# Optimization experiments

Measured on AMD Instinct MI355X. Metric: run time of the kernel, lower is better.

Reference implementation:

```python
import jax, jax.numpy as jnp
import numpy as np

VOCAB, EMB, HID = 32000, 512, 1024
BATCH, SEQ = 32, 512


def setup_inputs() -> dict:
    key = jax.random.key(0)
    ks = jax.random.split(key, 5)
    scale_e = 1.0 / np.sqrt(EMB)
    scale_h = 1.0 / np.sqrt(HID)
    return {
        "source": jax.random.randint(ks[0], (BATCH, SEQ), 0, VOCAB, dtype=jnp.int64),
        "embedding": jax.random.normal(ks[1], (VOCAB, EMB), dtype=jnp.float32),
        "W_ih": jax.random.normal(ks[2], (EMB, 4 * HID), dtype=jnp.float32) * scale_e,
        "W_hh": jax.random.normal(ks[3], (HID, 4 * HID), dtype=jnp.float32) * scale_h,
        "b_ih": jnp.zeros((4 * HID,), dtype=jnp.float32),
        "b_hh": jnp.zeros((4 * HID,), dtype=jnp.float32),
    }


def _lstm_forward(source, embedding, W_ih, W_hh, b_ih, b_hh):
    B, S = source.shape
    H = W_hh.shape[0]
    embedded = embedding[source]                      # [B, S, E]
    # Precompute input contributions for all timesteps in one big GEMM.
    x_gates = jnp.einsum("bse,eg->bsg", embedded, W_ih) + b_ih + b_hh  # [B, S, 4H]

    def step(carry, xg_t):
        h, c = carry
        gates = xg_t + h @ W_hh                       # [B, 4H]
        i, f, g, o = jnp.split(gates, 4, axis=-1)
        i = jax.nn.sigmoid(i)
        f = jax.nn.sigmoid(f)
        g = jnp.tanh(g)
        o = jax.nn.sigmoid(o)
        c_new = f * c + i * g
        h_new = o * jnp.tanh(c_new)
        return (h_new, c_new), h_new

    h0 = jnp.zeros((B, H), dtype=embedded.dtype)
    c0 = jnp.zeros((B, H), dtype=embedded.dtype)
    # scan over time: [S, B, 4H]
    _, hiddens = jax.lax.scan(step, (h0, c0), jnp.swapaxes(x_gates, 0, 1))
    return jnp.swapaxes(hiddens, 0, 1)                # [B, S, H]


def reference(source, embedding, W_ih, W_hh, b_ih, b_hh):
    return _lstm_forward(source, embedding, W_ih, W_hh, b_ih, b_hh)
```

## Files before the change

### kernel.cpp

```cpp
#include <hip/hip_runtime.h>
#include <math.h>


#define B_ 32
#define S_ 512
#define E_ 512
#define H_ 1024
#define G_ 4096
#define NWG 256
#define RTHR 512
#define BH_ (B_ * H_)
#define XGPAD 40

typedef _Float16 f16x8 __attribute__((ext_vector_type(8)));
typedef _Float16 f16x4 __attribute__((ext_vector_type(4)));
typedef float f32x4 __attribute__((ext_vector_type(4)));

__device__ __forceinline__ float sigmoidf_(float x) {
  return 1.0f / (1.0f + __expf(-x));
}
__device__ __forceinline__ float tanhf_(float x) {
  return 1.0f - 2.0f / (__expf(2.0f * x) + 1.0f);
}

__global__ __launch_bounds__(256) void wt_kernel(
    const float* __restrict__ W, _Float16* __restrict__ Wt, int K)
{
  __shared__ float Lt[64][65];
  const int c0 = blockIdx.x * 64;
  const int k0 = blockIdx.y * 64;
  const int tid = threadIdx.x;
  const int colL = tid & 63;
  const int rq = tid >> 6;
#pragma unroll 4
  for (int p = 0; p < 16; ++p) {
    int r = p * 4 + rq;
    Lt[colL][r] = W[(size_t)(k0 + r) * G_ + c0 + colL];
  }
  __syncthreads();
  const int col = tid >> 2;
  const int kq = (tid & 3) * 16;
  _Float16 tmp[16];
#pragma unroll
  for (int i = 0; i < 16; ++i) tmp[i] = (_Float16)Lt[col][kq + i];
  *(f16x8*)(Wt + (size_t)(c0 + col) * K + k0 + kq)     = *(f16x8*)&tmp[0];
  *(f16x8*)(Wt + (size_t)(c0 + col) * K + k0 + kq + 8) = *(f16x8*)&tmp[8];
}

__global__ __launch_bounds__(128) void gather_a(
    const int* __restrict__ src, const float* __restrict__ emb,
    _Float16* __restrict__ A, int t0)
{
  const int r = blockIdx.x;
  const int t = t0 + (r >> 5), b = r & 31;
  const int vrow = src[b * S_ + t];
  const float4 v = *(const float4*)(emb + (size_t)vrow * E_ + threadIdx.x * 4);
  f16x4 o = { (_Float16)v.x, (_Float16)v.y, (_Float16)v.z, (_Float16)v.w };
  *(f16x4*)(A + (size_t)r * E_ + threadIdx.x * 4) = o;
}

__global__ __launch_bounds__(256) void xgates_mfma(
    const _Float16* __restrict__ A, const _Float16* __restrict__ Bw,
    const float* __restrict__ bih, const float* __restrict__ bhh,
    _Float16* __restrict__ xg)
{
  __shared__ _Float16 Al[128][XGPAD];
  __shared__ _Float16 Bl[128][XGPAD];
  const int tid = threadIdx.x;
  const int row0 = blockIdx.y * 128;
  const int col0 = blockIdx.x * 128;
  const int wave = tid >> 6, lane = tid & 63;
  const int wm = wave >> 1, wn = wave & 1;
  const int lrow = lane & 15, lhi = lane >> 4;

  float bias[4];
#pragma unroll
  for (int n = 0; n < 4; ++n) {
    int c = col0 + wn * 64 + n * 16 + lrow;
    bias[n] = bih[c] + bhh[c];
  }
  f32x4 acc[4][4];
#pragma unroll
  for (int m = 0; m < 4; ++m)
#pragma unroll
    for (int n = 0; n < 4; ++n)
      acc[m][n] = (f32x4){bias[n], bias[n], bias[n], bias[n]};

  for (int kt = 0; kt < E_ / 32; ++kt) {
#pragma unroll
    for (int p = 0; p < 2; ++p) {
      int cch = tid * 2 + p;
      int rr = cch >> 2, kc = cch & 3;
      *(f16x8*)&Al[rr][kc * 8] =
          *(const f16x8*)(A + (size_t)(row0 + rr) * E_ + kt * 32 + kc * 8);
      *(f16x8*)&Bl[rr][kc * 8] =
          *(const f16x8*)(Bw + (size_t)(col0 + rr) * E_ + kt * 32 + kc * 8);
    }
    __syncthreads();
    f16x8 af[4], bfr[4];
#pragma unroll
    for (int m = 0; m < 4; ++m)
      af[m] = *(const f16x8*)&Al[wm * 64 + m * 16 + lrow][lhi * 8];
#pragma unroll
    for (int n = 0; n < 4; ++n)
      bfr[n] = *(const f16x8*)&Bl[wn * 64 + n * 16 + lrow][lhi * 8];
#pragma unroll
    for (int m = 0; m < 4; ++m)
#pragma unroll
      for (int n = 0; n < 4; ++n)
        acc[m][n] = __builtin_amdgcn_mfma_f32_16x16x32_f16(af[m], bfr[n],
                                                           acc[m][n], 0, 0, 0);
    __syncthreads();
  }
#pragma unroll
  for (int m = 0; m < 4; ++m)
#pragma unroll
    for (int n = 0; n < 4; ++n) {
      const int ccol = col0 + wn * 64 + n * 16 + lrow;
#pragma unroll
      for (int r = 0; r < 4; ++r) {
        const int rrow = row0 + wm * 64 + m * 16 + lhi * 4 + r;
        xg[(size_t)rrow * G_ + ccol] = (_Float16)acc[m][n][r];
      }
    }
}

__global__ __launch_bounds__(RTHR) void lstm_mfma(
    const _Float16* __restrict__ Wt, const _Float16* __restrict__ xg,
    unsigned short* hring, float* cbuf, unsigned* flg,
    float* out, int t0, int nt)
{
  __shared__ float red[8 * 32 * 17];

  const int wg = blockIdx.x;
  const int tid = threadIdx.x;
  const int J0 = 4 * ((wg & 7) * 32 + (wg >> 3));

  const int wave = tid >> 6;
  const int lane = tid & 63;
  const int lrow = lane & 15;
  const int lhi  = lane >> 4;
  const int Kw   = wave * 128;
  const int gcol = (lrow >> 2) * H_ + J0 + (lrow & 3);

  f16x8 bf[4];
#pragma unroll
  for (int s = 0; s < 4; ++s)
    bf[s] = *(const f16x8*)(Wt + (size_t)gcol * H_ + Kw + s * 32 + lhi * 8);

  const int bq = tid >> 2, jq = tid & 3;
  float cstate = 0.f;
  if (tid < 128) cstate = cbuf[(size_t)bq * H_ + J0 + jq];

  float xv0 = 0.f, xv1 = 0.f, xv2 = 0.f, xv3 = 0.f;
  if (tid < 128) {
    const _Float16* xp = xg + (size_t)bq * G_ + J0 + jq;
    xv0 = (float)xp[0];      xv1 = (float)xp[H_];
    xv2 = (float)xp[2 * H_]; xv3 = (float)xp[3 * H_];
  }

  for (int t = t0; t < t0 + nt; ++t) {
    const int lt = t - t0;
    const _Float16* hrd = (const _Float16*)hring + (size_t)lt * BH_;
    unsigned short* hwr = hring + (size_t)((lt == nt - 1) ? 0 : lt + 1) * BH_;

    if (wave == 0) {
      const unsigned* fp = flg + (size_t)t * 256 + lane * 4;
      int guard = 0;
      for (;;) {
        unsigned a0 = __hip_atomic_load(fp + 0, __ATOMIC_RELAXED, __HIP_MEMORY_SCOPE_AGENT);
        unsigned a1 = __hip_atomic_load(fp + 1, __ATOMIC_RELAXED, __HIP_MEMORY_SCOPE_AGENT);
        unsigned a2 = __hip_atomic_load(fp + 2, __ATOMIC_RELAXED, __HIP_MEMORY_SCOPE_AGENT);
        unsigned a3 = __hip_atomic_load(fp + 3, __ATOMIC_RELAXED, __HIP_MEMORY_SCOPE_AGENT);
        if (__all((a0 & a1 & a2 & a3) != 0u)) break;
        __builtin_amdgcn_s_sleep(1);
        if (++guard > (1 << 22)) break;
      }
    }
    __syncthreads();

    f32x4 acc0 = {0.f, 0.f, 0.f, 0.f};
    f32x4 acc1 = {0.f, 0.f, 0.f, 0.f};
#pragma unroll
    for (int s = 0; s < 4; ++s) {
      f16x8 a0 = *(const f16x8*)(hrd + (size_t)lrow * H_ + Kw + s * 32 + lhi * 8);
      f16x8 a1 = *(const f16x8*)(hrd + (size_t)(16 + lrow) * H_ + Kw + s * 32 + lhi * 8);
      acc0 = __builtin_amdgcn_mfma_f32_16x16x32_f16(a0, bf[s], acc0, 0, 0, 0);
      acc1 = __builtin_amdgcn_mfma_f32_16x16x32_f16(a1, bf[s], acc1, 0, 0, 0);
    }

    float xn0 = 0.f, xn1 = 0.f, xn2 = 0.f, xn3 = 0.f;
    if (tid < 128) {
      const int nlt = (lt == nt - 1) ? lt : lt + 1;
      const _Float16* xp = xg + ((size_t)nlt * B_ + bq) * G_ + J0 + jq;
      xn0 = (float)xp[0];      xn1 = (float)xp[H_];
      xn2 = (float)xp[2 * H_]; xn3 = (float)xp[3 * H_];
    }

#pragma unroll
    for (int r = 0; r < 4; ++r) {
      red[(wave * 32 + lhi * 4 + r) * 17 + lrow]      = acc0[r];
      red[(wave * 32 + 16 + lhi * 4 + r) * 17 + lrow] = acc1[r];
    }
    __syncthreads();

    if (tid < 128) {
      float g0 = xv0, g1 = xv1, g2 = xv2, g3 = xv3;
#pragma unroll
      for (int w = 0; w < 8; ++w) {
        const float* rp = red + (w * 32 + bq) * 17;
        g0 += rp[jq];
        g1 += rp[4 + jq];
        g2 += rp[8 + jq];
        g3 += rp[12 + jq];
      }
      float ig = sigmoidf_(g0);
      float fg = sigmoidf_(g1);
      float gg = tanhf_(g2);
      float og = sigmoidf_(g3);
      cstate = fg * cstate + ig * gg;
      float hval = og * tanhf_(cstate);
      out[((size_t)bq * S_ + t) * H_ + J0 + jq] = hval;
      _Float16 hf = (_Float16)hval;
      unsigned short hb;
      __builtin_memcpy(&hb, &hf, 2);
      __hip_atomic_store(hwr + (size_t)bq * H_ + J0 + jq, hb,
                         __ATOMIC_RELAXED, __HIP_MEMORY_SCOPE_AGENT);
    }
    __syncthreads();

    if (tid == 0)
      __hip_atomic_store(flg + (size_t)(t + 1) * 256 + wg, 1u,
                         __ATOMIC_RELAXED, __HIP_MEMORY_SCOPE_AGENT);

    xv0 = xn0; xv1 = xn1; xv2 = xn2; xv3 = xn3;
  }

  if (tid < 128) cbuf[(size_t)bq * H_ + J0 + jq] = cstate;
}

extern "C" void kernel_launch(void* const* d_in, const int* in_sizes, int n_in,
                              void* d_out, int out_size, void* d_ws, size_t ws_size,
                              hipStream_t stream) {
  const int*   src = (const int*)d_in[0];
  const float* emb = (const float*)d_in[1];
  const float* Wih = (const float*)d_in[2];
  const float* Whh = (const float*)d_in[3];
  const float* bih = (const float*)d_in[4];
  const float* bhh = (const float*)d_in[5];
  float* out = (float*)d_out;

  char* ws = (char*)d_ws;
  float*    cbuf = (float*)ws;
  unsigned* flg  = (unsigned*)(ws + 131072);
  const size_t stateBytes = 131072 + 525312;
  _Float16* Wt  = (_Float16*)(ws + stateBytes);
  _Float16* Wt2 = (_Float16*)(ws + stateBytes + 8388608);
  const size_t fixedBytes = stateBytes + 8388608 + 4194304;

  int chunk = 0;
  const int cand[4] = {512, 256, 128, 64};
  for (int ci = 0; ci < 4; ++ci) {
    size_t need = fixedBytes + (size_t)(cand[ci] + 1) * (BH_ * 2)
                  + (size_t)cand[ci] * B_ * E_ * 2
                  + (size_t)cand[ci] * B_ * G_ * 2;
    if (need <= ws_size) { chunk = cand[ci]; break; }
  }
  if (chunk == 0) return;

  unsigned short* hring = (unsigned short*)(ws + fixedBytes);
  _Float16* Af16 = (_Float16*)(ws + fixedBytes + (size_t)(chunk + 1) * (BH_ * 2));
  _Float16* xg   = (_Float16*)(ws + fixedBytes + (size_t)(chunk + 1) * (BH_ * 2)
                               + (size_t)chunk * B_ * E_ * 2);

  (void)hipMemsetAsync(ws, 0, stateBytes, stream);
  (void)hipMemsetAsync(flg, 1, 1024, stream);
  (void)hipMemsetAsync(hring, 0, BH_ * 2, stream);

  int K1 = H_, K2 = E_;
  wt_kernel<<<dim3(64, 16), 256, 0, stream>>>(Whh, Wt, K1);
  wt_kernel<<<dim3(64, 8), 256, 0, stream>>>(Wih, Wt2, K2);

  for (int t0 = 0; t0 < S_; t0 += chunk) {
    gather_a<<<dim3(chunk * B_), 128, 0, stream>>>(src, emb, Af16, t0);
    xgates_mfma<<<dim3(G_ / 128, chunk * B_ / 128), 256, 0, stream>>>(
        Af16, Wt2, bih, bhh, xg);

    int nt = chunk;
    void* args[] = {(void*)&Wt, (void*)&xg, (void*)&hring, (void*)&cbuf,
                    (void*)&flg, (void*)&out, (void*)&t0, (void*)&nt};
    (void)hipLaunchCooperativeKernel((void*)lstm_mfma, dim3(NWG), dim3(RTHR),
                                     args, 0u, stream);
  }
}
```

Measured before the change: 2.642 ms.

## Restructure recurrent LSTM kernel to per-wave full-K MFMA with wave-level flags

Replaces the 256-workgroup recurrent kernel, which split K across 8 waves and reduced through LDS with three block barriers per step, by a 64-workgroup layout. Each wave now owns a 16-batch by 4-hidden-unit tile over the full K=1024, holds 32 register fragments of W_hh, and combines gates through lane shuffles instead of shared memory. Synchronisation moves to per-wave flags split by batch half, so each wave waits only on the 256 producers of its batch half and signals independently, with no __syncthreads. This trades much higher register pressure and longer serial MFMA chains per wave for removing the block barriers and LDS reduction from the per-step critical path.

```diff
diff --git a/kernel.cpp b/kernel.cpp
--- a/kernel.cpp
+++ b/kernel.cpp
@@ -7,7 +7,7 @@
 #define E_ 512
 #define H_ 1024
 #define G_ 4096
-#define NWG 256
+#define NWG 64
 #define RTHR 512
 #define BH_ (B_ * H_)
 #define XGPAD 40
@@ -125,47 +125,41 @@
     }
 }
 
-__global__ __launch_bounds__(RTHR) void lstm_mfma(
+__global__ __launch_bounds__(RTHR) void lstm_wave(
     const _Float16* __restrict__ Wt, const _Float16* __restrict__ xg,
     unsigned short* hring, float* cbuf, unsigned* flg,
     float* out, int t0, int nt)
 {
-  __shared__ float red[8 * 32 * 17];
-
   const int wg = blockIdx.x;
   const int tid = threadIdx.x;
-  const int J0 = 4 * ((wg & 7) * 32 + (wg >> 3));
-
   const int wave = tid >> 6;
   const int lane = tid & 63;
-  const int lrow = lane & 15;
-  const int lhi  = lane >> 4;
-  const int Kw   = wave * 128;
-  const int gcol = (lrow >> 2) * H_ + J0 + (lrow & 3);
-
-  f16x8 bf[4];
-#pragma unroll
-  for (int s = 0; s < 4; ++s)
-    bf[s] = *(const f16x8*)(Wt + (size_t)gcol * H_ + Kw + s * 32 + lhi * 8);
-
-  const int bq = tid >> 2, jq = tid & 3;
-  float cstate = 0.f;
-  if (tid < 128) cstate = cbuf[(size_t)bq * H_ + J0 + jq];
-
-  float xv0 = 0.f, xv1 = 0.f, xv2 = 0.f, xv3 = 0.f;
-  if (tid < 128) {
-    const _Float16* xp = xg + (size_t)bq * G_ + J0 + jq;
-    xv0 = (float)xp[0];      xv1 = (float)xp[H_];
-    xv2 = (float)xp[2 * H_]; xv3 = (float)xp[3 * H_];
-  }
+  const int lrow = lane & 15, lhi = lane >> 4;
+  const int bt = wave >> 2;
+  const int ct = wave & 3;
+  const int gcol = (lrow >> 2) * H_ + wg * 16 + ct * 4 + (lrow & 3);
+
+  f16x8 bf[32];
+#pragma unroll
+  for (int s = 0; s < 32; ++s)
+    bf[s] = *(const f16x8*)(Wt + (size_t)gcol * H_ + s * 32 + lhi * 8);
+
+  const int ej    = lane & 3;
+  const int ersel = (lane >> 2) & 3;
+  const int ebl   = (lane >> 4) * 4 + ersel;
+  const int eb    = bt * 16 + ebl;
+  const int eu    = wg * 16 + ct * 4 + ej;
+  const int shbase = (lane & 48) | ej;
+
+  float cstate = cbuf[(size_t)eb * H_ + eu];
 
   for (int t = t0; t < t0 + nt; ++t) {
     const int lt = t - t0;
     const _Float16* hrd = (const _Float16*)hring + (size_t)lt * BH_;
     unsigned short* hwr = hring + (size_t)((lt == nt - 1) ? 0 : lt + 1) * BH_;
 
-    if (wave == 0) {
-      const unsigned* fp = flg + (size_t)t * 256 + lane * 4;
+    {
+      const unsigned* fp = flg + (size_t)t * 512 + bt * 256 + lane * 4;
       int guard = 0;
       for (;;) {
         unsigned a0 = __hip_atomic_load(fp + 0, __ATOMIC_RELAXED, __HIP_MEMORY_SCOPE_AGENT);
@@ -174,69 +168,67 @@
         unsigned a3 = __hip_atomic_load(fp + 3, __ATOMIC_RELAXED, __HIP_MEMORY_SCOPE_AGENT);
         if (__all((a0 & a1 & a2 & a3) != 0u)) break;
         __builtin_amdgcn_s_sleep(1);
-        if (++guard > (1 << 22)) break;
+        if (++guard > (1 << 20)) break;
       }
     }
-    __syncthreads();
-
-    f32x4 acc0 = {0.f, 0.f, 0.f, 0.f};
-    f32x4 acc1 = {0.f, 0.f, 0.f, 0.f};
-#pragma unroll
-    for (int s = 0; s < 4; ++s) {
-      f16x8 a0 = *(const f16x8*)(hrd + (size_t)lrow * H_ + Kw + s * 32 + lhi * 8);
-      f16x8 a1 = *(const f16x8*)(hrd + (size_t)(16 + lrow) * H_ + Kw + s * 32 + lhi * 8);
-      acc0 = __builtin_amdgcn_mfma_f32_16x16x32_f16(a0, bf[s], acc0, 0, 0, 0);
-      acc1 = __builtin_amdgcn_mfma_f32_16x16x32_f16(a1, bf[s], acc1, 0, 0, 0);
-    }
-
-    float xn0 = 0.f, xn1 = 0.f, xn2 = 0.f, xn3 = 0.f;
-    if (tid < 128) {
-      const int nlt = (lt == nt - 1) ? lt : lt + 1;
-      const _Float16* xp = xg + ((size_t)nlt * B_ + bq) * G_ + J0 + jq;
-      xn0 = (float)xp[0];      xn1 = (float)xp[H_];
-      xn2 = (float)xp[2 * H_]; xn3 = (float)xp[3 * H_];
-    }
-
-#pragma unroll
-    for (int r = 0; r < 4; ++r) {
-      red[(wave * 32 + lhi * 4 + r) * 17 + lrow]      = acc0[r];
-      red[(wave * 32 + 16 + lhi * 4 + r) * 17 + lrow] = acc1[r];
-    }
-    __syncthreads();
-
-    if (tid < 128) {
-      float g0 = xv0, g1 = xv1, g2 = xv2, g3 = xv3;
-#pragma unroll
-      for (int w = 0; w < 8; ++w) {
-        const float* rp = red + (w * 32 + bq) * 17;
-        g0 += rp[jq];
-        g1 += rp[4 + jq];
-        g2 += rp[8 + jq];
-        g3 += rp[12 + jq];
-      }
-      float ig = sigmoidf_(g0);
-      float fg = sigmoidf_(g1);
-      float gg = tanhf_(g2);
-      float og = sigmoidf_(g3);
-      cstate = fg * cstate + ig * gg;
-      float hval = og * tanhf_(cstate);
-      out[((size_t)bq * S_ + t) * H_ + J0 + jq] = hval;
-      _Float16 hf = (_Float16)hval;
-      unsigned short hb;
-      __builtin_memcpy(&hb, &hf, 2);
-      __hip_atomic_store(hwr + (size_t)bq * H_ + J0 + jq, hb,
-                         __ATOMIC_RELAXED, __HIP_MEMORY_SCOPE_AGENT);
-    }
-    __syncthreads();
-
-    if (tid == 0)
-      __hip_atomic_store(flg + (size_t)(t + 1) * 256 + wg, 1u,
-                         __ATOMIC_RELAXED, __HIP_MEMORY_SCOPE_AGENT);
-
-    xv0 = xn0; xv1 = xn1; xv2 = xn2; xv3 = xn3;
-  }
-
-  if (tid < 128) cbuf[(size_t)bq * H_ + J0 + jq] = cstate;
+
+    const _Float16* xp = xg + ((size_t)lt * B_ + eb) * G_ + eu;
+    const float x0 = (float)xp[0];
+    const float x1 = (float)xp[H_];
+    const float x2 = (float)xp[2 * H_];
+    const float x3 = (float)xp[3 * H_];
+
+    const _Float16* hp = hrd + (size_t)(bt * 16 + lrow) * H_ + lhi * 8;
+    f32x4 acA = {0.f, 0.f, 0.f, 0.f};
+    f32x4 acB = {0.f, 0.f, 0.f, 0.f};
+#pragma unroll
+    for (int sb = 0; sb < 8; ++sb) {
+      f16x8 a0 = *(const f16x8*)(hp + (sb * 4 + 0) * 32);
+      f16x8 a1 = *(const f16x8*)(hp + (sb * 4 + 1) * 32);
+      f16x8 a2 = *(const f16x8*)(hp + (sb * 4 + 2) * 32);
+      f16x8 a3 = *(const f16x8*)(hp + (sb * 4 + 3) * 32);
+      acA = __builtin_amdgcn_mfma_f32_16x16x32_f16(a0, bf[sb * 4 + 0], acA, 0, 0, 0);
+      acB = __builtin_amdgcn_mfma_f32_16x16x32_f16(a1, bf[sb * 4 + 1], acB, 0, 0, 0);
+      acA = __builtin_amdgcn_mfma_f32_16x16x32_f16(a2, bf[sb * 4 + 2], acA, 0, 0, 0);
+      acB = __builtin_amdgcn_mfma_f32_16x16x32_f16(a3, bf[sb * 4 + 3], acB, 0, 0, 0);
+    }
+    const float av0 = acA[0] + acB[0];
+    const float av1 = acA[1] + acB[1];
+    const float av2 = acA[2] + acB[2];
+    const float av3 = acA[3] + acB[3];
+
+    float gv[4];
+#pragma unroll
+    for (int g = 0; g < 4; ++g) {
+      const int srcl = shbase + g * 4;
+      const float t0v = __shfl(av0, srcl);
+      const float t1v = __shfl(av1, srcl);
+      const float t2v = __shfl(av2, srcl);
+      const float t3v = __shfl(av3, srcl);
+      gv[g] = (ersel == 0) ? t0v : (ersel == 1) ? t1v : (ersel == 2) ? t2v : t3v;
+    }
+
+    const float ig = sigmoidf_(x0 + gv[0]);
+    const float fg = sigmoidf_(x1 + gv[1]);
+    const float gg = tanhf_(x2 + gv[2]);
+    const float og = sigmoidf_(x3 + gv[3]);
+    cstate = fg * cstate + ig * gg;
+    const float hval = og * tanhf_(cstate);
+
+    out[((size_t)eb * S_ + t) * H_ + eu] = hval;
+    const _Float16 hf = (_Float16)hval;
+    unsigned short hb;
+    __builtin_memcpy(&hb, &hf, 2);
+    __hip_atomic_store(hwr + (size_t)eb * H_ + eu, hb,
+                       __ATOMIC_RELAXED, __HIP_MEMORY_SCOPE_AGENT);
+
+    asm volatile("s_waitcnt vmcnt(0)" ::: "memory");
+    if (lane == 0)
+      __hip_atomic_store(flg + (size_t)(t + 1) * 512 + bt * 256 + wg * 4 + ct,
+                         1u, __ATOMIC_RELAXED, __HIP_MEMORY_SCOPE_AGENT);
+  }
+
+  cbuf[(size_t)eb * H_ + eu] = cstate;
 }
 
 extern "C" void kernel_launch(void* const* d_in, const int* in_sizes, int n_in,
@@ -253,7 +245,7 @@
   char* ws = (char*)d_ws;
   float*    cbuf = (float*)ws;
   unsigned* flg  = (unsigned*)(ws + 131072);
-  const size_t stateBytes = 131072 + 525312;
+  const size_t stateBytes = 131072 + 1050624;
   _Float16* Wt  = (_Float16*)(ws + stateBytes);
   _Float16* Wt2 = (_Float16*)(ws + stateBytes + 8388608);
   const size_t fixedBytes = stateBytes + 8388608 + 4194304;
@@ -274,7 +266,7 @@
                                + (size_t)chunk * B_ * E_ * 2);
 
   (void)hipMemsetAsync(ws, 0, stateBytes, stream);
-  (void)hipMemsetAsync(flg, 1, 1024, stream);
+  (void)hipMemsetAsync(flg, 1, 2048, stream);
   (void)hipMemsetAsync(hring, 0, BH_ * 2, stream);
 
   int K1 = H_, K2 = E_;
@@ -289,7 +281,7 @@
     int nt = chunk;
     void* args[] = {(void*)&Wt, (void*)&xg, (void*)&hring, (void*)&cbuf,
                     (void*)&flg, (void*)&out, (void*)&t0, (void*)&nt};
-    (void)hipLaunchCooperativeKernel((void*)lstm_mfma, dim3(NWG), dim3(RTHR),
+    (void)hipLaunchCooperativeKernel((void*)lstm_wave, dim3(NWG), dim3(RTHR),
                                      args, 0u, stream);
   }
 }
```

Measured after the change: 9.898 ms. 275% more time.

## Replace per-step flag barrier with step-tagged hidden-state values in double buffer

Applied to the files above, without the earlier changes.

The recurrent kernel no longer uses a separate flag array and spin on per-workgroup flags. Instead each hidden value is stored as a 32-bit word carrying the fp16 value plus the timestep tag, in a two-slot buffer. Consumers spin directly on the data they need until every tag matches the current step. The work split also changes: each workgroup now handles 16 batch rows by 8 units rather than 32 rows by 4 units. This removes one flag round-trip and two block barriers per step, and lets the reads that confirm readiness double as the operand loads. In exchange each hidden load is twice as wide, and every lane polls 16 atomic words.

```diff
diff --git a/kernel.cpp b/kernel.cpp
--- a/kernel.cpp
+++ b/kernel.cpp
@@ -15,12 +15,16 @@
 typedef _Float16 f16x8 __attribute__((ext_vector_type(8)));
 typedef _Float16 f16x4 __attribute__((ext_vector_type(4)));
 typedef float f32x4 __attribute__((ext_vector_type(4)));
+typedef unsigned long long u64;
 
 __device__ __forceinline__ float sigmoidf_(float x) {
   return 1.0f / (1.0f + __expf(-x));
 }
 __device__ __forceinline__ float tanhf_(float x) {
   return 1.0f - 2.0f / (__expf(2.0f * x) + 1.0f);
+}
+__device__ __forceinline__ unsigned pack_(u64 q) {
+  return (unsigned)(q & 0xFFFFu) | ((unsigned)(q >> 16) & 0xFFFF0000u);
 }
 
 __global__ __launch_bounds__(256) void wt_kernel(
@@ -125,118 +129,133 @@
     }
 }
 
-__global__ __launch_bounds__(RTHR) void lstm_mfma(
+#define LDQ(i) q##i = __hip_atomic_load(                                    \
+    hq + (((i) >> 2) * 16 + ((i) & 3)), __ATOMIC_RELAXED,                   \
+    __HIP_MEMORY_SCOPE_AGENT);
+#define XOR8(a,b,c,d,e,f,g,h) (((a)|(b))|((c)|(d)))|(((e)|(f))|((g)|(h)))
+
+__global__ __launch_bounds__(RTHR, 2) void lstm_tag(
     const _Float16* __restrict__ Wt, const _Float16* __restrict__ xg,
-    unsigned short* hring, float* cbuf, unsigned* flg,
-    float* out, int t0, int nt)
+    unsigned* hbuf, float* cbuf, float* out, int t0, int nt)
 {
-  __shared__ float red[8 * 32 * 17];
+  __shared__ float red[2][8][16][33];
 
   const int wg = blockIdx.x;
   const int tid = threadIdx.x;
-  const int J0 = 4 * ((wg & 7) * 32 + (wg >> 3));
+  const int bt = wg >> 7;
+  const int ug = wg & 127;
+  const int U0 = ug * 8;
 
   const int wave = tid >> 6;
   const int lane = tid & 63;
-  const int lrow = lane & 15;
-  const int lhi  = lane >> 4;
-  const int Kw   = wave * 128;
-  const int gcol = (lrow >> 2) * H_ + J0 + (lrow & 3);
-
-  f16x8 bf[4];
-#pragma unroll
-  for (int s = 0; s < 4; ++s)
-    bf[s] = *(const f16x8*)(Wt + (size_t)gcol * H_ + Kw + s * 32 + lhi * 8);
-
-  const int bq = tid >> 2, jq = tid & 3;
+  const int lrow = lane & 15, lhi = lane >> 4;
+  const int kq = wave;
+
+  f16x8 bfr[2][4];
+#pragma unroll
+  for (int ct = 0; ct < 2; ++ct) {
+    const int c = ct * 16 + lrow;
+    const int gcol = (c >> 3) * H_ + U0 + (c & 7);
+#pragma unroll
+    for (int s = 0; s < 4; ++s)
+      bfr[ct][s] = *(const f16x8*)(Wt + (size_t)gcol * H_ + kq * 128 + s * 32 + lhi * 8);
+  }
+
+  const int bl = tid >> 3, ej = tid & 7;
+  const int eb = bt * 16 + bl;
+  const int eu = U0 + ej;
   float cstate = 0.f;
-  if (tid < 128) cstate = cbuf[(size_t)bq * H_ + J0 + jq];
+  if (tid < 128) cstate = cbuf[(size_t)eb * H_ + eu];
 
   float xv0 = 0.f, xv1 = 0.f, xv2 = 0.f, xv3 = 0.f;
   if (tid < 128) {
-    const _Float16* xp = xg + (size_t)bq * G_ + J0 + jq;
+    const _Float16* xp = xg + (size_t)eb * G_ + eu;
     xv0 = (float)xp[0];      xv1 = (float)xp[H_];
     xv2 = (float)xp[2 * H_]; xv3 = (float)xp[3 * H_];
   }
 
+  const size_t rowOff64 = (size_t)(bt * 16 + lrow) * (H_ / 2) + kq * 64 + lhi * 4;
+
   for (int t = t0; t < t0 + nt; ++t) {
     const int lt = t - t0;
-    const _Float16* hrd = (const _Float16*)hring + (size_t)lt * BH_;
-    unsigned short* hwr = hring + (size_t)((lt == nt - 1) ? 0 : lt + 1) * BH_;
-
-    if (wave == 0) {
-      const unsigned* fp = flg + (size_t)t * 256 + lane * 4;
+    const int slot = t & 1, nslot = slot ^ 1;
+    const u64* hq = (const u64*)hbuf + (size_t)slot * (BH_ / 2) + rowOff64;
+
+    u64 q0, q1, q2, q3, q4, q5, q6, q7, q8, q9, q10, q11, q12, q13, q14, q15;
+    {
+      const u64 expect = ((u64)(unsigned)t << 16) | ((u64)(unsigned)t << 48);
       int guard = 0;
       for (;;) {
-        unsigned a0 = __hip_atomic_load(fp + 0, __ATOMIC_RELAXED, __HIP_MEMORY_SCOPE_AGENT);
-        unsigned a1 = __hip_atomic_load(fp + 1, __ATOMIC_RELAXED, __HIP_MEMORY_SCOPE_AGENT);
-        unsigned a2 = __hip_atomic_load(fp + 2, __ATOMIC_RELAXED, __HIP_MEMORY_SCOPE_AGENT);
-        unsigned a3 = __hip_atomic_load(fp + 3, __ATOMIC_RELAXED, __HIP_MEMORY_SCOPE_AGENT);
-        if (__all((a0 & a1 & a2 & a3) != 0u)) break;
+        LDQ(0)  LDQ(1)  LDQ(2)  LDQ(3)  LDQ(4)  LDQ(5)  LDQ(6)  LDQ(7)
+        LDQ(8)  LDQ(9)  LDQ(10) LDQ(11) LDQ(12) LDQ(13) LDQ(14) LDQ(15)
+        const u64 bad =
+            (XOR8(q0 ^ expect, q1 ^ expect, q2 ^ expect, q3 ^ expect,
+                  q4 ^ expect, q5 ^ expect, q6 ^ expect, q7 ^ expect) |
+             XOR8(q8 ^ expect, q9 ^ expect, q10 ^ expect, q11 ^ expect,
+                  q12 ^ expect, q13 ^ expect, q14 ^ expect, q15 ^ expect)) &
+            0xFFFF0000FFFF0000ULL;
+        if (__all(bad == 0ULL)) break;
         __builtin_amdgcn_s_sleep(1);
-        if (++guard > (1 << 22)) break;
+        if (++guard > (1 << 20)) break;
       }
     }
-    __syncthreads();
 
     f32x4 acc0 = {0.f, 0.f, 0.f, 0.f};
     f32x4 acc1 = {0.f, 0.f, 0.f, 0.f};
-#pragma unroll
-    for (int s = 0; s < 4; ++s) {
-      f16x8 a0 = *(const f16x8*)(hrd + (size_t)lrow * H_ + Kw + s * 32 + lhi * 8);
-      f16x8 a1 = *(const f16x8*)(hrd + (size_t)(16 + lrow) * H_ + Kw + s * 32 + lhi * 8);
-      acc0 = __builtin_amdgcn_mfma_f32_16x16x32_f16(a0, bf[s], acc0, 0, 0, 0);
-      acc1 = __builtin_amdgcn_mfma_f32_16x16x32_f16(a1, bf[s], acc1, 0, 0, 0);
-    }
-
-    float xn0 = 0.f, xn1 = 0.f, xn2 = 0.f, xn3 = 0.f;
-    if (tid < 128) {
-      const int nlt = (lt == nt - 1) ? lt : lt + 1;
-      const _Float16* xp = xg + ((size_t)nlt * B_ + bq) * G_ + J0 + jq;
-      xn0 = (float)xp[0];      xn1 = (float)xp[H_];
-      xn2 = (float)xp[2 * H_]; xn3 = (float)xp[3 * H_];
-    }
+#define KSTEP(s, qa, qb, qc, qd)                                              \
+    {                                                                         \
+      unsigned pu[4] = { pack_(qa), pack_(qb), pack_(qc), pack_(qd) };        \
+      f16x8 av;                                                               \
+      __builtin_memcpy(&av, pu, 16);                                          \
+      acc0 = __builtin_amdgcn_mfma_f32_16x16x32_f16(av, bfr[0][s], acc0, 0, 0, 0); \
+      acc1 = __builtin_amdgcn_mfma_f32_16x16x32_f16(av, bfr[1][s], acc1, 0, 0, 0); \
+    }
+    KSTEP(0, q0, q1, q2, q3)
+    KSTEP(1, q4, q5, q6, q7)
+    KSTEP(2, q8, q9, q10, q11)
+    KSTEP(3, q12, q13, q14, q15)
+#undef KSTEP
 
 #pragma unroll
     for (int r = 0; r < 4; ++r) {
-      red[(wave * 32 + lhi * 4 + r) * 17 + lrow]      = acc0[r];
-      red[(wave * 32 + 16 + lhi * 4 + r) * 17 + lrow] = acc1[r];
+      red[slot][kq][lhi * 4 + r][lrow]      = acc0[r];
+      red[slot][kq][lhi * 4 + r][16 + lrow] = acc1[r];
     }
     __syncthreads();
 
     if (tid < 128) {
       float g0 = xv0, g1 = xv1, g2 = xv2, g3 = xv3;
 #pragma unroll
-      for (int w = 0; w < 8; ++w) {
-        const float* rp = red + (w * 32 + bq) * 17;
-        g0 += rp[jq];
-        g1 += rp[4 + jq];
-        g2 += rp[8 + jq];
-        g3 += rp[12 + jq];
+      for (int k8 = 0; k8 < 8; ++k8) {
+        const float* rp = &red[slot][k8][bl][0];
+        g0 += rp[ej];
+        g1 += rp[8 + ej];
+        g2 += rp[16 + ej];
+        g3 += rp[24 + ej];
       }
-      float ig = sigmoidf_(g0);
-      float fg = sigmoidf_(g1);
-      float gg = tanhf_(g2);
-      float og = sigmoidf_(g3);
+      const float ig = sigmoidf_(g0);
+      const float fg = sigmoidf_(g1);
+      const float gg = tanhf_(g2);
+      const float og = sigmoidf_(g3);
       cstate = fg * cstate + ig * gg;
-      float hval = og * tanhf_(cstate);
-      out[((size_t)bq * S_ + t) * H_ + J0 + jq] = hval;
-      _Float16 hf = (_Float16)hval;
+      const float hval = og * tanhf_(cstate);
+
+      const _Float16 hf = (_Float16)hval;
       unsigned short hb;
       __builtin_memcpy(&hb, &hf, 2);
-      __hip_atomic_store(hwr + (size_t)bq * H_ + J0 + jq, hb,
+      const unsigned hu = ((unsigned)(t + 1) << 16) | (unsigned)hb;
+      __hip_atomic_store(hbuf + (size_t)nslot * BH_ + (size_t)eb * H_ + eu, hu,
                          __ATOMIC_RELAXED, __HIP_MEMORY_SCOPE_AGENT);
-    }
-    __syncthreads();
-
-    if (tid == 0)
-      __hip_atomic_store(flg + (size_t)(t + 1) * 256 + wg, 1u,
-                         __ATOMIC_RELAXED, __HIP_MEMORY_SCOPE_AGENT);
-
-    xv0 = xn0; xv1 = xn1; xv2 = xn2; xv3 = xn3;
-  }
-
-  if (tid < 128) cbuf[(size_t)bq * H_ + J0 + jq] = cstate;
+      out[((size_t)eb * S_ + t) * H_ + eu] = hval;
+
+      const int nlt = (lt == nt - 1) ? lt : lt + 1;
+      const _Float16* xp = xg + ((size_t)nlt * B_ + eb) * G_ + eu;
+      xv0 = (float)xp[0];      xv1 = (float)xp[H_];
+      xv2 = (float)xp[2 * H_]; xv3 = (float)xp[3 * H_];
+    }
+  }
+
+  if (tid < 128) cbuf[(size_t)eb * H_ + eu] = cstate;
 }
 
 extern "C" void kernel_launch(void* const* d_in, const int* in_sizes, int n_in,
@@ -252,8 +271,8 @@
 
   char* ws = (char*)d_ws;
   float*    cbuf = (float*)ws;
-  unsigned* flg  = (unsigned*)(ws + 131072);
-  const size_t stateBytes = 131072 + 525312;
+  unsigned* hbuf = (unsigned*)(ws + 131072);
+  const size_t stateBytes = 131072 + 262144;
   _Float16* Wt  = (_Float16*)(ws + stateBytes);
   _Float16* Wt2 = (_Float16*)(ws + stateBytes + 8388608);
   const size_t fixedBytes = stateBytes + 8388608 + 4194304;
@@ -261,21 +280,16 @@
   int chunk = 0;
   const int cand[4] = {512, 256, 128, 64};
   for (int ci = 0; ci < 4; ++ci) {
-    size_t need = fixedBytes + (size_t)(cand[ci] + 1) * (BH_ * 2)
-                  + (size_t)cand[ci] * B_ * E_ * 2
+    size_t need = fixedBytes + (size_t)cand[ci] * B_ * E_ * 2
                   + (size_t)cand[ci] * B_ * G_ * 2;
     if (need <= ws_size) { chunk = cand[ci]; break; }
   }
   if (chunk == 0) return;
 
-  unsigned short* hring = (unsigned short*)(ws + fixedBytes);
-  _Float16* Af16 = (_Float16*)(ws + fixedBytes + (size_t)(chunk + 1) * (BH_ * 2));
-  _Float16* xg   = (_Float16*)(ws + fixedBytes + (size_t)(chunk + 1) * (BH_ * 2)
-                               + (size_t)chunk * B_ * E_ * 2);
+  _Float16* Af16 = (_Float16*)(ws + fixedBytes);
+  _Float16* xg   = (_Float16*)(ws + fixedBytes + (size_t)chunk * B_ * E_ * 2);
 
   (void)hipMemsetAsync(ws, 0, stateBytes, stream);
-  (void)hipMemsetAsync(flg, 1, 1024, stream);
-  (void)hipMemsetAsync(hring, 0, BH_ * 2, stream);
 
   int K1 = H_, K2 = E_;
   wt_kernel<<<dim3(64, 16), 256, 0, stream>>>(Whh, Wt, K1);
@@ -287,9 +301,9 @@
         Af16, Wt2, bih, bhh, xg);
 
     int nt = chunk;
-    void* args[] = {(void*)&Wt, (void*)&xg, (void*)&hring, (void*)&cbuf,
-                    (void*)&flg, (void*)&out, (void*)&t0, (void*)&nt};
-    (void)hipLaunchCooperativeKernel((void*)lstm_mfma, dim3(NWG), dim3(RTHR),
+    void* args[] = {(void*)&Wt, (void*)&xg, (void*)&hbuf, (void*)&cbuf,
+                    (void*)&out, (void*)&t0, (void*)&nt};
+    (void)hipLaunchCooperativeKernel((void*)lstm_tag, dim3(NWG), dim3(RTHR),
                                      args, 0u, stream);
   }
 }
```

Measured after the change: 5.486 ms. 2.08x slower.

## Split recurrent LSTM work by batch halves to narrow cross-workgroup flag waits

Applied to the files above, without the earlier changes.

Each workgroup now handles 16 batch rows and 8 hidden units (32 gate columns), not all 32 batch rows and 4 hidden units. This lets each workgroup wait only on the 128 flags of its own batch half instead of all 256. The W_hh fragments held in registers double, but each wave loads one h fragment per k-step and reuses it across two MFMAs. The next-step x-gate prefetch is also moved to after the h store, which shortens the critical path between flag wait and flag publish.

```diff
diff --git a/kernel.cpp b/kernel.cpp
--- a/kernel.cpp
+++ b/kernel.cpp
@@ -125,36 +125,43 @@
     }
 }
 
-__global__ __launch_bounds__(RTHR) void lstm_mfma(
+__global__ __launch_bounds__(RTHR) void lstm_half(
     const _Float16* __restrict__ Wt, const _Float16* __restrict__ xg,
     unsigned short* hring, float* cbuf, unsigned* flg,
     float* out, int t0, int nt)
 {
-  __shared__ float red[8 * 32 * 17];
+  __shared__ float red[8][16][33];
 
   const int wg = blockIdx.x;
   const int tid = threadIdx.x;
-  const int J0 = 4 * ((wg & 7) * 32 + (wg >> 3));
+  const int ht  = wg >> 7;
+  const int rem = wg & 127;
+  const int U0  = 8 * ((rem & 7) * 16 + (rem >> 3));
 
   const int wave = tid >> 6;
   const int lane = tid & 63;
-  const int lrow = lane & 15;
-  const int lhi  = lane >> 4;
-  const int Kw   = wave * 128;
-  const int gcol = (lrow >> 2) * H_ + J0 + (lrow & 3);
-
-  f16x8 bf[4];
-#pragma unroll
-  for (int s = 0; s < 4; ++s)
-    bf[s] = *(const f16x8*)(Wt + (size_t)gcol * H_ + Kw + s * 32 + lhi * 8);
-
-  const int bq = tid >> 2, jq = tid & 3;
+  const int lrow = lane & 15, lhi = lane >> 4;
+  const int kq = wave;
+
+  f16x8 bfr[2][4];
+#pragma unroll
+  for (int ct = 0; ct < 2; ++ct) {
+    const int c = ct * 16 + lrow;
+    const int gcol = (c >> 3) * H_ + U0 + (c & 7);
+#pragma unroll
+    for (int s = 0; s < 4; ++s)
+      bfr[ct][s] = *(const f16x8*)(Wt + (size_t)gcol * H_ + kq * 128 + s * 32 + lhi * 8);
+  }
+
+  const int bl = tid >> 3, ej = tid & 7;
+  const int eb = ht * 16 + bl;
+  const int eu = U0 + ej;
   float cstate = 0.f;
-  if (tid < 128) cstate = cbuf[(size_t)bq * H_ + J0 + jq];
+  if (tid < 128) cstate = cbuf[(size_t)eb * H_ + eu];
 
   float xv0 = 0.f, xv1 = 0.f, xv2 = 0.f, xv3 = 0.f;
   if (tid < 128) {
-    const _Float16* xp = xg + (size_t)bq * G_ + J0 + jq;
+    const _Float16* xp = xg + (size_t)eb * G_ + eu;
     xv0 = (float)xp[0];      xv1 = (float)xp[H_];
     xv2 = (float)xp[2 * H_]; xv3 = (float)xp[3 * H_];
   }
@@ -165,78 +172,74 @@
     unsigned short* hwr = hring + (size_t)((lt == nt - 1) ? 0 : lt + 1) * BH_;
 
     if (wave == 0) {
-      const unsigned* fp = flg + (size_t)t * 256 + lane * 4;
+      const unsigned* fp = flg + (size_t)t * 256 + ht * 128 + lane;
       int guard = 0;
       for (;;) {
-        unsigned a0 = __hip_atomic_load(fp + 0, __ATOMIC_RELAXED, __HIP_MEMORY_SCOPE_AGENT);
-        unsigned a1 = __hip_atomic_load(fp + 1, __ATOMIC_RELAXED, __HIP_MEMORY_SCOPE_AGENT);
-        unsigned a2 = __hip_atomic_load(fp + 2, __ATOMIC_RELAXED, __HIP_MEMORY_SCOPE_AGENT);
-        unsigned a3 = __hip_atomic_load(fp + 3, __ATOMIC_RELAXED, __HIP_MEMORY_SCOPE_AGENT);
-        if (__all((a0 & a1 & a2 & a3) != 0u)) break;
+        unsigned a0 = __hip_atomic_load(fp, __ATOMIC_RELAXED,
+                                        __HIP_MEMORY_SCOPE_AGENT);
+        unsigned a1 = __hip_atomic_load(fp + 64, __ATOMIC_RELAXED,
+                                        __HIP_MEMORY_SCOPE_AGENT);
+        if (__all((a0 & a1) != 0u)) break;
         __builtin_amdgcn_s_sleep(1);
         if (++guard > (1 << 22)) break;
       }
     }
     __syncthreads();
 
+    const _Float16* hp = hrd + (size_t)(ht * 16 + lrow) * H_ + kq * 128 + lhi * 8;
     f32x4 acc0 = {0.f, 0.f, 0.f, 0.f};
     f32x4 acc1 = {0.f, 0.f, 0.f, 0.f};
 #pragma unroll
     for (int s = 0; s < 4; ++s) {
-      f16x8 a0 = *(const f16x8*)(hrd + (size_t)lrow * H_ + Kw + s * 32 + lhi * 8);
-      f16x8 a1 = *(const f16x8*)(hrd + (size_t)(16 + lrow) * H_ + Kw + s * 32 + lhi * 8);
-      acc0 = __builtin_amdgcn_mfma_f32_16x16x32_f16(a0, bf[s], acc0, 0, 0, 0);
-      acc1 = __builtin_amdgcn_mfma_f32_16x16x32_f16(a1, bf[s], acc1, 0, 0, 0);
-    }
-
-    float xn0 = 0.f, xn1 = 0.f, xn2 = 0.f, xn3 = 0.f;
-    if (tid < 128) {
-      const int nlt = (lt == nt - 1) ? lt : lt + 1;
-      const _Float16* xp = xg + ((size_t)nlt * B_ + bq) * G_ + J0 + jq;
-      xn0 = (float)xp[0];      xn1 = (float)xp[H_];
-      xn2 = (float)xp[2 * H_]; xn3 = (float)xp[3 * H_];
+      const f16x8 av = *(const f16x8*)(hp + s * 32);
+      acc0 = __builtin_amdgcn_mfma_f32_16x16x32_f16(av, bfr[0][s], acc0, 0, 0, 0);
+      acc1 = __builtin_amdgcn_mfma_f32_16x16x32_f16(av, bfr[1][s], acc1, 0, 0, 0);
     }
 
 #pragma unroll
     for (int r = 0; r < 4; ++r) {
-      red[(wave * 32 + lhi * 4 + r) * 17 + lrow]      = acc0[r];
-      red[(wave * 32 + 16 + lhi * 4 + r) * 17 + lrow] = acc1[r];
+      red[kq][lhi * 4 + r][lrow]      = acc0[r];
+      red[kq][lhi * 4 + r][16 + lrow] = acc1[r];
     }
     __syncthreads();
 
     if (tid < 128) {
       float g0 = xv0, g1 = xv1, g2 = xv2, g3 = xv3;
 #pragma unroll
-      for (int w = 0; w < 8; ++w) {
-        const float* rp = red + (w * 32 + bq) * 17;
-        g0 += rp[jq];
-        g1 += rp[4 + jq];
-        g2 += rp[8 + jq];
-        g3 += rp[12 + jq];
+      for (int k8 = 0; k8 < 8; ++k8) {
+        const float* rp = &red[k8][bl][0];
+        g0 += rp[ej];
+        g1 += rp[8 + ej];
+        g2 += rp[16 + ej];
+        g3 += rp[24 + ej];
       }
-      float ig = sigmoidf_(g0);
-      float fg = sigmoidf_(g1);
-      float gg = tanhf_(g2);
-      float og = sigmoidf_(g3);
+      const float ig = sigmoidf_(g0);
+      const float fg = sigmoidf_(g1);
+      const float gg = tanhf_(g2);
+      const float og = sigmoidf_(g3);
       cstate = fg * cstate + ig * gg;
-      float hval = og * tanhf_(cstate);
-      out[((size_t)bq * S_ + t) * H_ + J0 + jq] = hval;
-      _Float16 hf = (_Float16)hval;
+      const float hval = og * tanhf_(cstate);
+
+      out[((size_t)eb * S_ + t) * H_ + eu] = hval;
+      const _Float16 hf = (_Float16)hval;
       unsigned short hb;
       __builtin_memcpy(&hb, &hf, 2);
-      __hip_atomic_store(hwr + (size_t)bq * H_ + J0 + jq, hb,
+      __hip_atomic_store(hwr + (size_t)eb * H_ + eu, hb,
                          __ATOMIC_RELAXED, __HIP_MEMORY_SCOPE_AGENT);
+
+      const int nlt = (lt == nt - 1) ? lt : lt + 1;
+      const _Float16* xp = xg + ((size_t)nlt * B_ + eb) * G_ + eu;
+      xv0 = (float)xp[0];      xv1 = (float)xp[H_];
+      xv2 = (float)xp[2 * H_]; xv3 = (float)xp[3 * H_];
     }
     __syncthreads();
 
     if (tid == 0)
-      __hip_atomic_store(flg + (size_t)(t + 1) * 256 + wg, 1u,
+      __hip_atomic_store(flg + (size_t)(t + 1) * 256 + ht * 128 + rem, 1u,
                          __ATOMIC_RELAXED, __HIP_MEMORY_SCOPE_AGENT);
-
-    xv0 = xn0; xv1 = xn1; xv2 = xn2; xv3 = xn3;
-  }
-
-  if (tid < 128) cbuf[(size_t)bq * H_ + J0 + jq] = cstate;
+  }
+
+  if (tid < 128) cbuf[(size_t)eb * H_ + eu] = cstate;
 }
 
 extern "C" void kernel_launch(void* const* d_in, const int* in_sizes, int n_in,
@@ -289,7 +292,7 @@
     int nt = chunk;
     void* args[] = {(void*)&Wt, (void*)&xg, (void*)&hring, (void*)&cbuf,
                     (void*)&flg, (void*)&out, (void*)&t0, (void*)&nt};
-    (void)hipLaunchCooperativeKernel((void*)lstm_mfma, dim3(NWG), dim3(RTHR),
+    (void)hipLaunchCooperativeKernel((void*)lstm_half, dim3(NWG), dim3(RTHR),
                                      args, 0u, stream);
   }
 }
```

Measured after the change: 3.166 ms. +19.8%, slower.
